# Optimization experiments

Measured on AMD Instinct MI355X. Metric: run time of the kernel, lower is better.

## Reference

```python
import jax, jax.numpy as jnp
import numpy as np

S = 64    # shapelets_size
N = 256   # num_shapelets
C = 3     # in_channels
B = 64
L = 2048


def setup_inputs() -> dict:
    key = jax.random.key(0)
    kx, ks = jax.random.split(key)
    x = jax.random.normal(kx, (B, C, L), dtype=jnp.float32)
    shapelets = jax.random.normal(ks, (C, N, S), dtype=jnp.float32)
    return {"x": x, "shapelets": shapelets}


def reference(x, shapelets):
    # x: (B, C, L); shapelets: (C, N, S)
    W = x.shape[2] - S + 1  # number of sliding windows
    # unfold: (B, C, W, S)
    idx = jnp.arange(W)[:, None] + jnp.arange(S)[None, :]
    win = x[:, :, idx]
    # cdist with mm-based euclidean: d^2 = |a|^2 + |b|^2 - 2 a.b
    win_sq = jnp.sum(win * win, axis=-1)                 # (B, C, W)
    shp_sq = jnp.sum(shapelets * shapelets, axis=-1)     # (C, N)
    cross = jnp.einsum('bcws,cns->bcwn', win, shapelets)  # (B, C, W, N)
    d2 = win_sq[..., None] + shp_sq[None, :, None, :] - 2.0 * cross
    d = jnp.sqrt(jnp.maximum(d2, 0.0))                   # (B, C, W, N)
    # sum over channels, keepdim -> (B, 1, W, N); transpose -> (B, 1, N, W); min over W
    summed = jnp.sum(d, axis=1, keepdims=True)
    out = jnp.min(jnp.swapaxes(summed, 2, 3), axis=3)    # (B, 1, N)
    return out
```

## Files before the change

kernel.cpp:

```cpp
#include <hip/hip_runtime.h>
#include <hip/hip_fp16.h>


typedef float  v4f __attribute__((ext_vector_type(4)));
typedef short  v8s __attribute__((ext_vector_type(8)));
typedef unsigned short u16;
typedef unsigned int   u32;
typedef unsigned long long u64;

#define S_ 64
#define N_ 256
#define C_ 3
#define B_ 64
#define L_ 2048
#define W_ 1985
#define NCHUNK 530
#define THREADS 512
#define WAVES 8

__device__ __forceinline__ u16 f2bf(float f) {
    u32 u = __builtin_bit_cast(u32, f);
    return (u16)((u + 0x7FFFu + ((u >> 16) & 1u)) >> 16);
}
__device__ __forceinline__ float bf2f(u16 b) {
    return __builtin_bit_cast(float, ((u32)b) << 16);
}

__global__ __launch_bounds__(THREADS, 2)
void shapelet_min_kernel(const float* __restrict__ x,
                         const float* __restrict__ shp,
                         float* __restrict__ out)
{
    __shared__ u64 xcopy[C_][4][NCHUNK];
    __shared__ __half wsq[C_][L_];
    __shared__ float red[WAVES][64];

    const int tid  = threadIdx.x;
    const int wave = tid >> 6;
    const int lane = tid & 63;
    const int m    = lane & 15;
    const int q    = lane >> 4;
    const int b    = blockIdx.x >> 2;
    const int n0   = (blockIdx.x & 3) << 6;

    u16* scratch = (u16*)&xcopy[0][0][0];
    #pragma unroll
    for (int k = 0; k < 6; ++k) {
        int idx = tid + k * THREADS;
        int sq = idx & 15;
        int n  = (idx >> 4) & 63;
        int c  = idx >> 10;
        v4f v = *(const v4f*)(shp + ((size_t)(c * N_ + n0 + n) * S_ + (sq << 2)));
        u64 pk = (u64)f2bf(v[0]) | ((u64)f2bf(v[1]) << 16)
               | ((u64)f2bf(v[2]) << 32) | ((u64)f2bf(v[3]) << 48);
        *(u64*)(scratch + ((c * 64 + n) * 72 + (sq << 2))) = pk;
    }
    __syncthreads();

    v8s bfr[C_][4][2];
    float ssq[C_][4];
    #pragma unroll
    for (int c = 0; c < C_; ++c) {
        #pragma unroll
        for (int nt = 0; nt < 4; ++nt) {
            float sacc = 0.f;
            #pragma unroll
            for (int h = 0; h < 2; ++h) {
                v8s f = *(const v8s*)(scratch + ((c * 64 + nt * 16 + m) * 72 + h * 32 + q * 8));
                bfr[c][nt][h] = f;
                #pragma unroll
                for (int j = 0; j < 8; ++j) {
                    float e = bf2f((u16)f[j]);
                    sacc += e * e;
                }
            }
            sacc += __shfl_xor(sacc, 16);
            sacc += __shfl_xor(sacc, 32);
            ssq[c][nt] = sacc;
        }
    }
    __syncthreads();

    {
        const float* xb = x + (size_t)b * (C_ * L_);
        #pragma unroll
        for (int k = 0; k < 4; ++k) {
            int gi = tid + k * THREADS;
            if (gi < C_ * NCHUNK) {
                int c = gi / NCHUNK;
                int t = gi - c * NCHUNK;
                int e = t << 2;
                float f[4];
                if (e + 3 < L_) {
                    v4f v = *(const v4f*)(xb + c * L_ + e);
                    f[0] = v[0]; f[1] = v[1]; f[2] = v[2]; f[3] = v[3];
                } else {
                    #pragma unroll
                    for (int i = 0; i < 4; ++i)
                        f[i] = (e + i < L_) ? xb[c * L_ + e + i] : 0.f;
                }
                u16 u[4];
                #pragma unroll
                for (int i = 0; i < 4; ++i) u[i] = f2bf(f[i]);
                #pragma unroll
                for (int r = 0; r < 4; ++r) {
                    u16* cp = (u16*)&xcopy[c][r][0];
                    #pragma unroll
                    for (int i = 0; i < 4; ++i) {
                        int pos = e + i - r;
                        if (pos >= 0) cp[pos] = u[i];
                    }
                }
            }
        }
    }
    __syncthreads();

    #pragma unroll
    for (int c = 0; c < C_; ++c) {
        const u64* cp0 = &xcopy[c][0][0];
        float e[68];
        #pragma unroll
        for (int kk = 0; kk < 17; ++kk) {
            u64 ch = cp0[tid + kk];
            e[kk * 4 + 0] = bf2f((u16)(ch));
            e[kk * 4 + 1] = bf2f((u16)(ch >> 16));
            e[kk * 4 + 2] = bf2f((u16)(ch >> 32));
            e[kk * 4 + 3] = bf2f((u16)(ch >> 48));
        }
        float s0 = 0.f;
        #pragma unroll
        for (int i = 0; i < 64; ++i) s0 += e[i] * e[i];
        float s1 = s0 - e[0] * e[0] + e[64] * e[64];
        float s2 = s1 - e[1] * e[1] + e[65] * e[65];
        float s3 = s2 - e[2] * e[2] + e[66] * e[66];
        union { u64 u; __half h[4]; } hp;
        hp.h[0] = __float2half(s0); hp.h[1] = __float2half(s1);
        hp.h[2] = __float2half(s2); hp.h[3] = __float2half(s3);
        *(u64*)&wsq[c][tid << 2] = hp.u;
    }
    __syncthreads();

    float mins[4] = {1e30f, 1e30f, 1e30f, 1e30f};
    const int r = m & 3;

    #pragma unroll 1
    for (int it = 0; it < 8; ++it) {
        const int wbase = it * 256 + wave * 32;
        if (wbase >= W_) continue;

        float sums[2][4][4];
        #pragma unroll
        for (int mt = 0; mt < 2; ++mt)
            #pragma unroll
            for (int nt = 0; nt < 4; ++nt)
                #pragma unroll
                for (int g = 0; g < 4; ++g) sums[mt][nt][g] = 0.f;

        #pragma unroll
        for (int c = 0; c < C_; ++c) {
            v8s afr[2][2];
            #pragma unroll
            for (int mt = 0; mt < 2; ++mt) {
                #pragma unroll
                for (int h = 0; h < 2; ++h) {
                    int p0 = wbase + mt * 16 + m + h * 32 + q * 8;
                    int T  = (p0 - r) >> 2;
                    const u64* cp = &xcopy[c][r][0];
                    union { u64 u[2]; v8s v; } tmp;
                    tmp.u[0] = cp[T];
                    tmp.u[1] = cp[T + 1];
                    afr[mt][h] = tmp.v;
                }
            }
            v4f acc[2][4];
            #pragma unroll
            for (int mt = 0; mt < 2; ++mt)
                #pragma unroll
                for (int nt = 0; nt < 4; ++nt)
                    acc[mt][nt] = (v4f){0.f, 0.f, 0.f, 0.f};

            #pragma unroll
            for (int h = 0; h < 2; ++h)
                #pragma unroll
                for (int mt = 0; mt < 2; ++mt)
                    #pragma unroll
                    for (int nt = 0; nt < 4; ++nt)
                        acc[mt][nt] = __builtin_amdgcn_mfma_f32_16x16x32_bf16(
                            afr[mt][h], bfr[c][nt][h], acc[mt][nt], 0, 0, 0);

            #pragma unroll
            for (int mt = 0; mt < 2; ++mt) {
                union { u64 u; __half h4[4]; } wq;
                wq.u = *(const u64*)&wsq[c][wbase + mt * 16 + q * 4];
                float wv[4];
                #pragma unroll
                for (int g = 0; g < 4; ++g) wv[g] = __half2float(wq.h4[g]);
                #pragma unroll
                for (int nt = 0; nt < 4; ++nt) {
                    #pragma unroll
                    for (int g = 0; g < 4; ++g) {
                        float d2 = wv[g] + ssq[c][nt] - 2.f * acc[mt][nt][g];
                        d2 = fmaxf(d2, 0.f);
                        sums[mt][nt][g] += __builtin_amdgcn_sqrtf(d2);
                    }
                }
            }
        }
        #pragma unroll
        for (int mt = 0; mt < 2; ++mt) {
            #pragma unroll
            for (int g = 0; g < 4; ++g) {
                int w = wbase + mt * 16 + q * 4 + g;
                bool ok = (w < W_);
                #pragma unroll
                for (int nt = 0; nt < 4; ++nt) {
                    float vv = ok ? sums[mt][nt][g] : 1e30f;
                    mins[nt] = fminf(mins[nt], vv);
                }
            }
        }
    }

    #pragma unroll
    for (int nt = 0; nt < 4; ++nt) {
        mins[nt] = fminf(mins[nt], __shfl_xor(mins[nt], 16));
        mins[nt] = fminf(mins[nt], __shfl_xor(mins[nt], 32));
    }
    if (lane < 16) {
        #pragma unroll
        for (int nt = 0; nt < 4; ++nt) red[wave][nt * 16 + lane] = mins[nt];
    }
    __syncthreads();
    if (tid < 64) {
        float v = red[0][tid];
        #pragma unroll
        for (int wv = 1; wv < WAVES; ++wv) v = fminf(v, red[wv][tid]);
        out[(size_t)b * N_ + n0 + tid] = v;
    }
}

extern "C" void kernel_launch(void* const* d_in, const int* in_sizes, int n_in,
                              void* d_out, int out_size, void* d_ws, size_t ws_size,
                              hipStream_t stream) {
    const float* x   = (const float*)d_in[0];
    const float* shp = (const float*)d_in[1];
    float* out       = (float*)d_out;
    hipLaunchKernelGGL(shapelet_min_kernel, dim3(256), dim3(THREADS), 0, stream,
                       x, shp, out);
}
```

Measured before the change: 85.47 us.

## Double block size, split shapelet tiles across wave pairs, fold distance terms into MFMA accumulator

Raises the block to 1024 threads and splits each block's 64 shapelets between wave pairs, so every wave holds only 2 shapelet tiles in registers. The -2 factor is folded into the bf16 window copy, and the MFMA accumulator is seeded with window and shapelet squared norms, which removes the per-element fixup arithmetic. To keep the norms consistent, the window squared sums are computed from the scaled copy and multiplied by 0.25. Global x loads are issued before the shapelet fragment setup so their latency overlaps it, and the reduction buffer reuses the wsq shared memory. In exchange, each block's x preprocessing and shapelet norm work is still done once but spread over more waves, and occupancy now depends on the register and LDS budget of 1024-thread blocks.

Result: no change. 85.60 us (+0.1%).

```diff
diff --git a/kernel.cpp b/kernel.cpp
--- a/kernel.cpp
+++ b/kernel.cpp
@@ -15,8 +15,8 @@
 #define L_ 2048
 #define W_ 1985
 #define NCHUNK 530
-#define THREADS 512
-#define WAVES 8
+#define THREADS 1024
+#define WAVES 16
 
 __device__ __forceinline__ u16 f2bf(float f) {
     u32 u = __builtin_bit_cast(u32, f);
@@ -26,26 +26,27 @@
     return __builtin_bit_cast(float, ((u32)b) << 16);
 }
 
-__global__ __launch_bounds__(THREADS, 2)
+__global__ __launch_bounds__(THREADS)
 void shapelet_min_kernel(const float* __restrict__ x,
                          const float* __restrict__ shp,
                          float* __restrict__ out)
 {
     __shared__ u64 xcopy[C_][4][NCHUNK];
     __shared__ __half wsq[C_][L_];
-    __shared__ float red[WAVES][64];
 
     const int tid  = threadIdx.x;
     const int wave = tid >> 6;
     const int lane = tid & 63;
     const int m    = lane & 15;
     const int q    = lane >> 4;
+    const int ww   = wave >> 1;
+    const int wn   = wave & 1;
     const int b    = blockIdx.x >> 2;
     const int n0   = (blockIdx.x & 3) << 6;
 
     u16* scratch = (u16*)&xcopy[0][0][0];
     #pragma unroll
-    for (int k = 0; k < 6; ++k) {
+    for (int k = 0; k < 3; ++k) {
         int idx = tid + k * THREADS;
         int sq = idx & 15;
         int n  = (idx >> 4) & 63;
@@ -57,16 +58,41 @@
     }
     __syncthreads();
 
-    v8s bfr[C_][4][2];
-    float ssq[C_][4];
+    const float* xb = x + (size_t)b * (C_ * L_);
+    float xf[2][8];
+    int xc[2], xt[2];
+    #pragma unroll
+    for (int k = 0; k < 2; ++k) {
+        int u = tid + k * THREADS;
+        bool act = (u < C_ * NCHUNK);
+        int uu = act ? u : 0;
+        int c = uu / NCHUNK;
+        int t = uu - c * NCHUNK;
+        int e = t << 2;
+        xc[k] = c; xt[k] = t;
+        if (act && (e + 7 < L_)) {
+            v4f a0 = *(const v4f*)(xb + c * L_ + e);
+            v4f a1 = *(const v4f*)(xb + c * L_ + e + 4);
+            xf[k][0] = a0[0]; xf[k][1] = a0[1]; xf[k][2] = a0[2]; xf[k][3] = a0[3];
+            xf[k][4] = a1[0]; xf[k][5] = a1[1]; xf[k][6] = a1[2]; xf[k][7] = a1[3];
+        } else {
+            #pragma unroll
+            for (int i = 0; i < 8; ++i)
+                xf[k][i] = (act && (e + i < L_)) ? xb[c * L_ + e + i] : 0.f;
+        }
+    }
+
+    v8s bfr[C_][2][2];
+    float ssq[C_][2];
     #pragma unroll
     for (int c = 0; c < C_; ++c) {
         #pragma unroll
-        for (int nt = 0; nt < 4; ++nt) {
+        for (int nt = 0; nt < 2; ++nt) {
             float sacc = 0.f;
             #pragma unroll
             for (int h = 0; h < 2; ++h) {
-                v8s f = *(const v8s*)(scratch + ((c * 64 + nt * 16 + m) * 72 + h * 32 + q * 8));
+                v8s f = *(const v8s*)(scratch +
+                         ((c * 64 + wn * 32 + nt * 16 + m) * 72 + h * 32 + q * 8));
                 bfr[c][nt][h] = f;
                 #pragma unroll
                 for (int j = 0; j < 8; ++j) {
@@ -81,79 +107,68 @@
     }
     __syncthreads();
 
-    {
-        const float* xb = x + (size_t)b * (C_ * L_);
-        #pragma unroll
-        for (int k = 0; k < 4; ++k) {
-            int gi = tid + k * THREADS;
-            if (gi < C_ * NCHUNK) {
-                int c = gi / NCHUNK;
-                int t = gi - c * NCHUNK;
-                int e = t << 2;
-                float f[4];
-                if (e + 3 < L_) {
-                    v4f v = *(const v4f*)(xb + c * L_ + e);
-                    f[0] = v[0]; f[1] = v[1]; f[2] = v[2]; f[3] = v[3];
-                } else {
-                    #pragma unroll
-                    for (int i = 0; i < 4; ++i)
-                        f[i] = (e + i < L_) ? xb[c * L_ + e + i] : 0.f;
-                }
-                u16 u[4];
-                #pragma unroll
-                for (int i = 0; i < 4; ++i) u[i] = f2bf(f[i]);
-                #pragma unroll
-                for (int r = 0; r < 4; ++r) {
-                    u16* cp = (u16*)&xcopy[c][r][0];
-                    #pragma unroll
-                    for (int i = 0; i < 4; ++i) {
-                        int pos = e + i - r;
-                        if (pos >= 0) cp[pos] = u[i];
-                    }
-                }
-            }
-        }
-    }
-    __syncthreads();
-
-    #pragma unroll
-    for (int c = 0; c < C_; ++c) {
-        const u64* cp0 = &xcopy[c][0][0];
-        float e[68];
-        #pragma unroll
-        for (int kk = 0; kk < 17; ++kk) {
-            u64 ch = cp0[tid + kk];
-            e[kk * 4 + 0] = bf2f((u16)(ch));
-            e[kk * 4 + 1] = bf2f((u16)(ch >> 16));
-            e[kk * 4 + 2] = bf2f((u16)(ch >> 32));
-            e[kk * 4 + 3] = bf2f((u16)(ch >> 48));
-        }
-        float s0 = 0.f;
-        #pragma unroll
-        for (int i = 0; i < 64; ++i) s0 += e[i] * e[i];
-        float s1 = s0 - e[0] * e[0] + e[64] * e[64];
-        float s2 = s1 - e[1] * e[1] + e[65] * e[65];
-        float s3 = s2 - e[2] * e[2] + e[66] * e[66];
-        union { u64 u; __half h[4]; } hp;
-        hp.h[0] = __float2half(s0); hp.h[1] = __float2half(s1);
-        hp.h[2] = __float2half(s2); hp.h[3] = __float2half(s3);
-        *(u64*)&wsq[c][tid << 2] = hp.u;
-    }
-    __syncthreads();
-
-    float mins[4] = {1e30f, 1e30f, 1e30f, 1e30f};
+    #pragma unroll
+    for (int k = 0; k < 2; ++k) {
+        int u = tid + k * THREADS;
+        if (u < C_ * NCHUNK) {
+            u16 w8[8];
+            #pragma unroll
+            for (int i = 0; i < 8; ++i) w8[i] = f2bf(-2.f * xf[k][i]);
+            #pragma unroll
+            for (int r = 0; r < 4; ++r) {
+                u64 pk = (u64)w8[r] | ((u64)w8[r + 1] << 16)
+                       | ((u64)w8[r + 2] << 32) | ((u64)w8[r + 3] << 48);
+                xcopy[xc[k]][r][xt[k]] = pk;
+            }
+        }
+    }
+    __syncthreads();
+
+    #pragma unroll
+    for (int k = 0; k < 2; ++k) {
+        int u = tid + k * THREADS;
+        if (u < 512 * C_) {
+            int c  = u >> 9;
+            int t0 = u & 511;
+            const u64* cp0 = &xcopy[c][0][0];
+            u64 ch = cp0[t0];
+            float h0 = bf2f((u16)ch),         h1 = bf2f((u16)(ch >> 16)),
+                  h2 = bf2f((u16)(ch >> 32)), h3 = bf2f((u16)(ch >> 48));
+            float s = h0 * h0 + h1 * h1 + h2 * h2 + h3 * h3;
+            #pragma unroll
+            for (int kk = 1; kk < 16; ++kk) {
+                u64 c2 = cp0[t0 + kk];
+                float e0 = bf2f((u16)c2),         e1 = bf2f((u16)(c2 >> 16)),
+                      e2 = bf2f((u16)(c2 >> 32)), e3 = bf2f((u16)(c2 >> 48));
+                s += e0 * e0; s += e1 * e1; s += e2 * e2; s += e3 * e3;
+            }
+            u64 ct = cp0[t0 + 16];
+            float t4 = bf2f((u16)ct), t5 = bf2f((u16)(ct >> 16)), t6 = bf2f((u16)(ct >> 32));
+            float s0 = s;
+            float s1 = s0 - h0 * h0 + t4 * t4;
+            float s2 = s1 - h1 * h1 + t5 * t5;
+            float s3 = s2 - h2 * h2 + t6 * t6;
+            union { u64 u; __half h[4]; } hp;
+            hp.h[0] = __float2half(0.25f * s0); hp.h[1] = __float2half(0.25f * s1);
+            hp.h[2] = __float2half(0.25f * s2); hp.h[3] = __float2half(0.25f * s3);
+            *(u64*)&wsq[c][t0 << 2] = hp.u;
+        }
+    }
+    __syncthreads();
+
+    float mins[2] = {1e30f, 1e30f};
     const int r = m & 3;
 
     #pragma unroll 1
     for (int it = 0; it < 8; ++it) {
-        const int wbase = it * 256 + wave * 32;
+        const int wbase = it * 256 + ww * 32;
         if (wbase >= W_) continue;
 
-        float sums[2][4][4];
+        float sums[2][2][4];
         #pragma unroll
         for (int mt = 0; mt < 2; ++mt)
             #pragma unroll
-            for (int nt = 0; nt < 4; ++nt)
+            for (int nt = 0; nt < 2; ++nt)
                 #pragma unroll
                 for (int g = 0; g < 4; ++g) sums[mt][nt][g] = 0.f;
 
@@ -173,22 +188,7 @@
                     afr[mt][h] = tmp.v;
                 }
             }
-            v4f acc[2][4];
-            #pragma unroll
-            for (int mt = 0; mt < 2; ++mt)
-                #pragma unroll
-                for (int nt = 0; nt < 4; ++nt)
-                    acc[mt][nt] = (v4f){0.f, 0.f, 0.f, 0.f};
-
-            #pragma unroll
-            for (int h = 0; h < 2; ++h)
-                #pragma unroll
-                for (int mt = 0; mt < 2; ++mt)
-                    #pragma unroll
-                    for (int nt = 0; nt < 4; ++nt)
-                        acc[mt][nt] = __builtin_amdgcn_mfma_f32_16x16x32_bf16(
-                            afr[mt][h], bfr[c][nt][h], acc[mt][nt], 0, 0, 0);
-
+            v4f acc[2][2];
             #pragma unroll
             for (int mt = 0; mt < 2; ++mt) {
                 union { u64 u; __half h4[4]; } wq;
@@ -197,45 +197,67 @@
                 #pragma unroll
                 for (int g = 0; g < 4; ++g) wv[g] = __half2float(wq.h4[g]);
                 #pragma unroll
-                for (int nt = 0; nt < 4; ++nt) {
-                    #pragma unroll
-                    for (int g = 0; g < 4; ++g) {
-                        float d2 = wv[g] + ssq[c][nt] - 2.f * acc[mt][nt][g];
-                        d2 = fmaxf(d2, 0.f);
-                        sums[mt][nt][g] += __builtin_amdgcn_sqrtf(d2);
-                    }
+                for (int nt = 0; nt < 2; ++nt)
+                    #pragma unroll
+                    for (int g = 0; g < 4; ++g)
+                        acc[mt][nt][g] = wv[g] + ssq[c][nt];
+            }
+            #pragma unroll
+            for (int h = 0; h < 2; ++h)
+                #pragma unroll
+                for (int mt = 0; mt < 2; ++mt)
+                    #pragma unroll
+                    for (int nt = 0; nt < 2; ++nt)
+                        acc[mt][nt] = __builtin_amdgcn_mfma_f32_16x16x32_bf16(
+                            afr[mt][h], bfr[c][nt][h], acc[mt][nt], 0, 0, 0);
+
+            #pragma unroll
+            for (int mt = 0; mt < 2; ++mt)
+                #pragma unroll
+                for (int nt = 0; nt < 2; ++nt)
+                    #pragma unroll
+                    for (int g = 0; g < 4; ++g)
+                        sums[mt][nt][g] += __builtin_amdgcn_sqrtf(fmaxf(acc[mt][nt][g], 0.f));
+        }
+
+        if (wbase + 31 < W_) {
+            #pragma unroll
+            for (int mt = 0; mt < 2; ++mt)
+                #pragma unroll
+                for (int nt = 0; nt < 2; ++nt)
+                    #pragma unroll
+                    for (int g = 0; g < 4; ++g)
+                        mins[nt] = fminf(mins[nt], sums[mt][nt][g]);
+        } else {
+            #pragma unroll
+            for (int mt = 0; mt < 2; ++mt)
+                #pragma unroll
+                for (int g = 0; g < 4; ++g) {
+                    int w = wbase + mt * 16 + q * 4 + g;
+                    bool ok = (w < W_);
+                    #pragma unroll
+                    for (int nt = 0; nt < 2; ++nt)
+                        mins[nt] = fminf(mins[nt], ok ? sums[mt][nt][g] : 1e30f);
                 }
-            }
-        }
-        #pragma unroll
-        for (int mt = 0; mt < 2; ++mt) {
-            #pragma unroll
-            for (int g = 0; g < 4; ++g) {
-                int w = wbase + mt * 16 + q * 4 + g;
-                bool ok = (w < W_);
-                #pragma unroll
-                for (int nt = 0; nt < 4; ++nt) {
-                    float vv = ok ? sums[mt][nt][g] : 1e30f;
-                    mins[nt] = fminf(mins[nt], vv);
-                }
-            }
-        }
-    }
-
-    #pragma unroll
-    for (int nt = 0; nt < 4; ++nt) {
+        }
+    }
+
+    #pragma unroll
+    for (int nt = 0; nt < 2; ++nt) {
         mins[nt] = fminf(mins[nt], __shfl_xor(mins[nt], 16));
         mins[nt] = fminf(mins[nt], __shfl_xor(mins[nt], 32));
     }
+    __syncthreads();
+    float* red = (float*)&wsq[0][0];
     if (lane < 16) {
-        #pragma unroll
-        for (int nt = 0; nt < 4; ++nt) red[wave][nt * 16 + lane] = mins[nt];
+        red[ww * 64 + wn * 32 + lane]      = mins[0];
+        red[ww * 64 + wn * 32 + 16 + lane] = mins[1];
     }
     __syncthreads();
     if (tid < 64) {
-        float v = red[0][tid];
-        #pragma unroll
-        for (int wv = 1; wv < WAVES; ++wv) v = fminf(v, red[wv][tid]);
+        float v = red[tid];
+        #pragma unroll
+        for (int k = 1; k < 8; ++k) v = fminf(v, red[k * 64 + tid]);
         out[(size_t)b * N_ + n0 + tid] = v;
     }
 }
```
